# Optimization experiments

Measured on AMD Instinct MI355X. Metric: run time of the kernel, lower is better.

Reference implementation:

```python
import jax, jax.numpy as jnp
import numpy as np

N = 500_000   # mesh vertices
M = 500_000   # non-manifold sample points
K = 4         # quad-mesh valence
WEIGHTS = [7000.0, 600.0, 10.0, 50.0, 30.0, 3.0]


def setup_inputs() -> dict:
    key = jax.random.key(0)
    ks = jax.random.split(key, 11)
    return {
        "manifold_pred": jax.random.normal(ks[0], (1, N), jnp.float32),
        "nonmanifold_pred": jax.random.normal(ks[1], (1, M), jnp.float32),
        "mnfld_grad": jax.random.normal(ks[2], (1, N, 3), jnp.float32),
        "nonmnfld_grad": jax.random.normal(ks[3], (1, M, 3), jnp.float32),
        "mnfld_hessian": jax.random.normal(ks[4], (1, N, 3, 3), jnp.float32),
        "mnfld_n_gt": jax.random.normal(ks[5], (1, N, 3), jnp.float32),
        "theta": jax.random.normal(ks[6], (1, N, 1), jnp.float32),
        "local_coord_u": jax.random.normal(ks[7], (1, N, 3), jnp.float32),
        "local_coord_v": jax.random.normal(ks[8], (1, N, 3), jnp.float32),
        "rot": jax.random.normal(ks[9], (N, K, 3, 3), jnp.float32),
        "neighbors": jax.random.randint(ks[10], (N, K), 0, N, jnp.int32),
    }


def reference(manifold_pred, nonmanifold_pred, mnfld_grad, nonmnfld_grad,
              mnfld_hessian, mnfld_n_gt, theta, local_coord_u, local_coord_v,
              rot, neighbors):
    H = mnfld_hessian[0]          # [N,3,3] per-vertex hessian
    n_gt = mnfld_n_gt[0]          # [N,3]

    # morse term: n^T H  (div_type == 'l1')
    morse = 0.5 * jnp.abs(jnp.einsum('nd,nde->ne', n_gt, H)).mean()

    sdf_term = jnp.abs(manifold_pred).mean()

    # eikonal over concatenated grads (morse path uses nonmnfld_grad when near_points is None)
    all_grads = jnp.concatenate([nonmnfld_grad, mnfld_grad], axis=-2)  # [1, M+N, 3]
    eikonal_term = jnp.abs(jnp.linalg.norm(all_grads, axis=2) - 1.0).mean()

    inter_term = jnp.exp(-100.0 * jnp.abs(nonmanifold_pred)).mean()

    # cross-field directions from theta
    u, v, th = local_coord_u[0], local_coord_v[0], theta[0]  # [N,3],[N,3],[N,1]
    va = u * jnp.cos(th) + v * jnp.sin(th)
    va = va / (jnp.linalg.norm(va, axis=-1, keepdims=True) + 1e-12)
    vb = -u * jnp.sin(th) + v * jnp.cos(th)
    vb = vb / (jnp.linalg.norm(vb, axis=-1, keepdims=True) + 1e-12)

    # per-vertex (v^T H) x v hessian alignment (single valence group covers all vertices)
    vaH = jnp.einsum('nd,nde->ne', va, H)
    vbH = jnp.einsum('nd,nde->ne', vb, H)
    h_alpha = jnp.abs(jnp.cross(vaH, va)).mean()
    h_beta = jnp.abs(jnp.cross(vbH, vb)).mean()
    theta_hessian_term = 0.5 * (h_alpha + h_beta)

    # neighbor consistency: rotate neighbor cross-field into vertex frame, dot products
    vaj = jnp.einsum('nkij,nkj->nki', rot, va[neighbors])  # [N,K,3]
    vbj = jnp.einsum('nkij,nkj->nki', rot, vb[neighbors])
    aa = jnp.abs(jnp.einsum('nd,nkd->nk', va, vaj))
    ab = jnp.abs(jnp.einsum('nd,nkd->nk', va, vbj))
    ba = jnp.abs(jnp.einsum('nd,nkd->nk', vb, vaj))
    bb = jnp.abs(jnp.einsum('nd,nkd->nk', vb, vbj))
    theta_neighbors_term = (aa + ab + ba + bb - 2.0).mean()

    w = WEIGHTS
    loss = (w[0] * sdf_term + w[1] * inter_term + w[3] * eikonal_term
            + w[5] * morse + w[2] * theta_hessian_term + w[4] * theta_neighbors_term)
    return jnp.stack([loss, sdf_term, inter_term, eikonal_term, morse,
                      theta_hessian_term, theta_neighbors_term])
```

## Files before the change

kernel.cpp:

```cpp
#include <hip/hip_runtime.h>
#include <math.h>

static constexpr int BLOCK = 256;
static constexpr int WAVES = BLOCK / 64;
static constexpr int KVAL = 4;
static constexpr int TILE = 512;

typedef float f4 __attribute__((ext_vector_type(4)));
typedef int i4 __attribute__((ext_vector_type(4)));
typedef unsigned int u4v __attribute__((ext_vector_type(4)));
union VV { u4v u4; _Float16 h[8]; };
union PQ { u4v u[3]; _Float16 h[24]; };

__device__ __forceinline__ void norm3(float x, float y, float z,
                                      float& ox, float& oy, float& oz) {
  float inv = 1.0f / (sqrtf(x * x + y * y + z * z) + 1e-12f);
  ox = x * inv; oy = y * inv; oz = z * inv;
}

template <int NV>
__device__ __forceinline__ void block_reduce(float (&p)[NV]) {
#pragma unroll
  for (int off = 32; off > 0; off >>= 1)
#pragma unroll
    for (int q = 0; q < NV; ++q) p[q] += __shfl_down(p[q], off, 64);
  __shared__ float sm[WAVES][NV];
  int wave = threadIdx.x >> 6, lane = threadIdx.x & 63;
  if (lane == 0)
#pragma unroll
    for (int q = 0; q < NV; ++q) sm[wave][q] = p[q];
  __syncthreads();
  if (threadIdx.x == 0) {
#pragma unroll
    for (int q = 0; q < NV; ++q) {
      float t = 0.f;
#pragma unroll
      for (int w = 1; w < WAVES; ++w) t += sm[w][q];
      p[q] += t;
    }
  }
}

__device__ __forceinline__ void stage_f(float* __restrict__ dst,
                                        const float* __restrict__ src, int nf) {
  int t = threadIdx.x;
  int nf4 = nf >> 2;
  const f4* s4 = (const f4*)src;
  f4* d4 = (f4*)dst;
  for (int i = t; i < nf4; i += BLOCK) d4[i] = s4[i];
  int rem = nf & 3;
  if (t < rem) dst[nf4 * 4 + t] = src[nf4 * 4 + t];
}

__global__ __launch_bounds__(BLOCK) void s1_kernel(
    const float* __restrict__ theta, const float* __restrict__ u,
    const float* __restrict__ v, u4v* __restrict__ vavb,
    u4v* __restrict__ pq0, u4v* __restrict__ pq1, u4v* __restrict__ pq2, int N,
    const float* __restrict__ pred, const float* __restrict__ pgrad,
    const float* __restrict__ mp, const float* __restrict__ grad,
    const float* __restrict__ H, const float* __restrict__ ngt,
    const float* __restrict__ rot,
    float* __restrict__ part1, int nb1, int M) {
  __shared__ float B[9216];
  int t = threadIdx.x;
  long base = (long)blockIdx.x * TILE;
  float p[5] = {0.f, 0.f, 0.f, 0.f, 0.f};

  int cntM = 0, cntN = 0;
  if (base < M) { long c = (long)M - base; cntM = c > TILE ? TILE : (int)c; }
  if (base < N) { long c = (long)N - base; cntN = c > TILE ? TILE : (int)c; }

  if (cntM > 0) stage_f(B, pgrad + 3 * base, 3 * cntM);
  if (cntN > 0) {
    stage_f(B + 1536, grad + 3 * base, 3 * cntN);
    stage_f(B + 3072, ngt + 3 * base, 3 * cntN);
  }
  __syncthreads();
  float ngt_r[2][3];
#pragma unroll
  for (int w = 0; w < 2; ++w) {
    int k = t + 256 * w;
    long i = base + k;
    if (k < cntM) {
      float gx = B[3 * k], gy = B[3 * k + 1], gz = B[3 * k + 2];
      p[1] += fabsf(sqrtf(gx * gx + gy * gy + gz * gz) - 1.0f);
      p[4] += __expf(-100.0f * fabsf(pred[i]));
    }
    if (k < cntN) {
      float gx = B[1536 + 3 * k], gy = B[1536 + 3 * k + 1], gz = B[1536 + 3 * k + 2];
      p[1] += fabsf(sqrtf(gx * gx + gy * gy + gz * gz) - 1.0f);
      p[0] += fabsf(mp[i]);
      ngt_r[w][0] = B[3072 + 3 * k];
      ngt_r[w][1] = B[3072 + 3 * k + 1];
      ngt_r[w][2] = B[3072 + 3 * k + 2];
    }
  }
  __syncthreads();

  if (cntN > 0) {
    stage_f(B, u + 3 * base, 3 * cntN);
    stage_f(B + 1536, v + 3 * base, 3 * cntN);
  }
  __syncthreads();
  float va_r[2][3], vb_r[2][3];
#pragma unroll
  for (int w = 0; w < 2; ++w) {
    int k = t + 256 * w;
    long i = base + k;
    if (k < cntN) {
      float s, c;
      __sincosf(theta[i], &s, &c);
      float ux = B[3 * k], uy = B[3 * k + 1], uz = B[3 * k + 2];
      float vx = B[1536 + 3 * k], vy = B[1536 + 3 * k + 1], vz = B[1536 + 3 * k + 2];
      norm3(ux * c + vx * s, uy * c + vy * s, uz * c + vz * s,
            va_r[w][0], va_r[w][1], va_r[w][2]);
      norm3(vx * c - ux * s, vy * c - uy * s, vz * c - uz * s,
            vb_r[w][0], vb_r[w][1], vb_r[w][2]);
      VV o;
      o.h[0] = (_Float16)va_r[w][0]; o.h[1] = (_Float16)va_r[w][1];
      o.h[2] = (_Float16)va_r[w][2];
      o.h[3] = (_Float16)vb_r[w][0]; o.h[4] = (_Float16)vb_r[w][1];
      o.h[5] = (_Float16)vb_r[w][2];
      o.h[6] = (_Float16)0.f; o.h[7] = (_Float16)0.f;
      vavb[i] = o.u4;
    }
  }
  __syncthreads();

  if (cntN > 0) stage_f(B, H + 9 * base, 9 * cntN);
  __syncthreads();
#pragma unroll
  for (int w = 0; w < 2; ++w) {
    int k = t + 256 * w;
    if (k < cntN) {
      float h[9];
#pragma unroll
      for (int q = 0; q < 9; ++q) h[q] = B[9 * k + q];
      float n0 = ngt_r[w][0], n1 = ngt_r[w][1], n2 = ngt_r[w][2];
      p[2] += fabsf(n0 * h[0] + n1 * h[3] + n2 * h[6]) +
              fabsf(n0 * h[1] + n1 * h[4] + n2 * h[7]) +
              fabsf(n0 * h[2] + n1 * h[5] + n2 * h[8]);
      const float* va = va_r[w];
      const float* vb = vb_r[w];
      float a0 = va[0] * h[0] + va[1] * h[3] + va[2] * h[6];
      float a1 = va[0] * h[1] + va[1] * h[4] + va[2] * h[7];
      float a2 = va[0] * h[2] + va[1] * h[5] + va[2] * h[8];
      float b0 = vb[0] * h[0] + vb[1] * h[3] + vb[2] * h[6];
      float b1 = vb[0] * h[1] + vb[1] * h[4] + vb[2] * h[7];
      float b2 = vb[0] * h[2] + vb[1] * h[5] + vb[2] * h[8];
      p[3] += fabsf(a1 * va[2] - a2 * va[1]) + fabsf(a2 * va[0] - a0 * va[2]) +
              fabsf(a0 * va[1] - a1 * va[0]) + fabsf(b1 * vb[2] - b2 * vb[1]) +
              fabsf(b2 * vb[0] - b0 * vb[2]) + fabsf(b0 * vb[1] - b1 * vb[0]);
    }
  }
  __syncthreads();

#pragma unroll
  for (int sp = 0; sp < 2; ++sp) {
    int cnt = cntN - 256 * sp;
    if (cnt > 256) cnt = 256;
    long sb = base + 256 * sp;
    if (cnt > 0) stage_f(B, rot + 36 * sb, 36 * cnt);
    __syncthreads();
    if (t < cnt) {
      long i = sb + t;
      const f4* rr = (const f4*)(B + 36 * t);
      float r[36];
#pragma unroll
      for (int q = 0; q < 9; ++q) {
        f4 x = rr[q];
        r[4 * q] = x.x; r[4 * q + 1] = x.y; r[4 * q + 2] = x.z; r[4 * q + 3] = x.w;
      }
      const float* va = va_r[sp];
      const float* vb = vb_r[sp];
      PQ o;
#pragma unroll
      for (int k = 0; k < KVAL; ++k) {
        const float* R = r + 9 * k;
#pragma unroll
        for (int j = 0; j < 3; ++j) {
          float pa = R[j] * va[0] + R[3 + j] * va[1] + R[6 + j] * va[2];
          float pb = R[j] * vb[0] + R[3 + j] * vb[1] + R[6 + j] * vb[2];
          o.h[6 * k + j] = (_Float16)pa;
          o.h[6 * k + 3 + j] = (_Float16)pb;
        }
      }
      pq0[i] = o.u[0]; pq1[i] = o.u[1]; pq2[i] = o.u[2];
    }
    __syncthreads();
  }

  block_reduce<5>(p);
  if (t == 0) {
#pragma unroll
    for (int q = 0; q < 5; ++q) part1[q * nb1 + blockIdx.x] = p[q];
  }
}

__global__ __launch_bounds__(BLOCK) void s3_kernel(
    const u4v* __restrict__ vavb, const u4v* __restrict__ pq0,
    const u4v* __restrict__ pq1, const u4v* __restrict__ pq2,
    const i4* __restrict__ nbr, float* __restrict__ part2, int N) {
  int n = blockIdx.x * BLOCK + threadIdx.x;
  float p[1] = {0.f};
  if (n < N) {
    i4 jj = nbr[n];
    int js[4] = {jj.x, jj.y, jj.z, jj.w};
    VV wn[4];
#pragma unroll
    for (int k = 0; k < KVAL; ++k) wn[k].u4 = vavb[js[k]];
    PQ o;
    o.u[0] = pq0[n]; o.u[1] = pq1[n]; o.u[2] = pq2[n];
    float nsum = 0.f;
#pragma unroll
    for (int k = 0; k < KVAL; ++k) {
      float pa0 = (float)o.h[6 * k],     pa1 = (float)o.h[6 * k + 1],
            pa2 = (float)o.h[6 * k + 2];
      float pb0 = (float)o.h[6 * k + 3], pb1 = (float)o.h[6 * k + 4],
            pb2 = (float)o.h[6 * k + 5];
      float aj0 = (float)wn[k].h[0], aj1 = (float)wn[k].h[1], aj2 = (float)wn[k].h[2];
      float bj0 = (float)wn[k].h[3], bj1 = (float)wn[k].h[4], bj2 = (float)wn[k].h[5];
      nsum += fabsf(pa0 * aj0 + pa1 * aj1 + pa2 * aj2) +
              fabsf(pa0 * bj0 + pa1 * bj1 + pa2 * bj2) +
              fabsf(pb0 * aj0 + pb1 * aj1 + pb2 * aj2) +
              fabsf(pb0 * bj0 + pb1 * bj1 + pb2 * bj2) - 2.0f;
    }
    p[0] = nsum;
  }
  block_reduce<1>(p);
  if (threadIdx.x == 0) part2[blockIdx.x] = p[0];
}

__global__ __launch_bounds__(BLOCK) void finalize_fast(
    const float* __restrict__ part1, int nb1, const float* __restrict__ part2,
    int nb2, float* __restrict__ out, int N, int M) {
  float s[6] = {0.f, 0.f, 0.f, 0.f, 0.f, 0.f};
  for (int b = threadIdx.x; b < nb1; b += BLOCK) {
#pragma unroll
    for (int q = 0; q < 5; ++q) s[q] += part1[q * nb1 + b];
  }
  for (int b = threadIdx.x; b < nb2; b += BLOCK) s[5] += part2[b];
  block_reduce<6>(s);
  if (threadIdx.x == 0) {
    float sdf = s[0] / (float)N;
    float eik = s[1] / (float)(N + M);
    float morse = 0.5f * s[2] / (3.0f * (float)N);
    float th = 0.5f * s[3] / (3.0f * (float)N);
    float inter = s[4] / (float)M;
    float nb = s[5] / ((float)N * (float)KVAL);
    float loss = 7000.0f * sdf + 600.0f * inter + 50.0f * eik + 3.0f * morse +
                 10.0f * th + 30.0f * nb;
    out[0] = loss; out[1] = sdf; out[2] = inter; out[3] = eik;
    out[4] = morse; out[5] = th; out[6] = nb;
  }
}

__device__ __forceinline__ void crossfield(const float* __restrict__ u,
                                           const float* __restrict__ v,
                                           const float* __restrict__ theta,
                                           int n, float va[3], float vb[3]) {
  float s, c;
  __sincosf(theta[n], &s, &c);
  float ux = u[3 * n], uy = u[3 * n + 1], uz = u[3 * n + 2];
  float vx = v[3 * n], vy = v[3 * n + 1], vz = v[3 * n + 2];
  norm3(ux * c + vx * s, uy * c + vy * s, uz * c + vz * s, va[0], va[1], va[2]);
  norm3(vx * c - ux * s, vy * c - uy * s, vz * c - uz * s, vb[0], vb[1], vb[2]);
}

__global__ __launch_bounds__(BLOCK) void vertex_kernel(
    const float* __restrict__ mp, const float* __restrict__ grad,
    const float* __restrict__ H, const float* __restrict__ ngt,
    const float* __restrict__ theta, const float* __restrict__ u,
    const float* __restrict__ v, const float* __restrict__ rot,
    const int* __restrict__ nbr, float* __restrict__ acc, int N) {
  int n = blockIdx.x * blockDim.x + threadIdx.x;
  float p[5] = {0.f, 0.f, 0.f, 0.f, 0.f};
  if (n < N) {
    float hh[9];
#pragma unroll
    for (int i = 0; i < 9; ++i) hh[i] = H[9 * (size_t)n + i];
    p[0] = fabsf(mp[n]);
    float gx = grad[3 * n], gy = grad[3 * n + 1], gz = grad[3 * n + 2];
    p[1] = fabsf(sqrtf(gx * gx + gy * gy + gz * gz) - 1.0f);
    float n0 = ngt[3 * n], n1 = ngt[3 * n + 1], n2 = ngt[3 * n + 2];
    p[2] = fabsf(n0 * hh[0] + n1 * hh[3] + n2 * hh[6]) +
           fabsf(n0 * hh[1] + n1 * hh[4] + n2 * hh[7]) +
           fabsf(n0 * hh[2] + n1 * hh[5] + n2 * hh[8]);
    float va[3], vb[3];
    crossfield(u, v, theta, n, va, vb);
    {
      float a0 = va[0] * hh[0] + va[1] * hh[3] + va[2] * hh[6];
      float a1 = va[0] * hh[1] + va[1] * hh[4] + va[2] * hh[7];
      float a2 = va[0] * hh[2] + va[1] * hh[5] + va[2] * hh[8];
      float b0 = vb[0] * hh[0] + vb[1] * hh[3] + vb[2] * hh[6];
      float b1 = vb[0] * hh[1] + vb[1] * hh[4] + vb[2] * hh[7];
      float b2 = vb[0] * hh[2] + vb[1] * hh[5] + vb[2] * hh[8];
      p[3] = fabsf(a1 * va[2] - a2 * va[1]) + fabsf(a2 * va[0] - a0 * va[2]) +
             fabsf(a0 * va[1] - a1 * va[0]) + fabsf(b1 * vb[2] - b2 * vb[1]) +
             fabsf(b2 * vb[0] - b0 * vb[2]) + fabsf(b0 * vb[1] - b1 * vb[0]);
    }
    float nsum = 0.f;
    const float* R = rot + (size_t)n * (KVAL * 9);
#pragma unroll
    for (int k = 0; k < KVAL; ++k) {
      int j = nbr[KVAL * (size_t)n + k];
      float vaj[3], vbj[3];
      crossfield(u, v, theta, j, vaj, vbj);
      float r0 = R[9 * k + 0], r1 = R[9 * k + 1], r2 = R[9 * k + 2];
      float r3 = R[9 * k + 3], r4 = R[9 * k + 4], r5 = R[9 * k + 5];
      float r6 = R[9 * k + 6], r7 = R[9 * k + 7], r8 = R[9 * k + 8];
      float wa0 = r0 * vaj[0] + r1 * vaj[1] + r2 * vaj[2];
      float wa1 = r3 * vaj[0] + r4 * vaj[1] + r5 * vaj[2];
      float wa2 = r6 * vaj[0] + r7 * vaj[1] + r8 * vaj[2];
      float wb0 = r0 * vbj[0] + r1 * vbj[1] + r2 * vbj[2];
      float wb1 = r3 * vbj[0] + r4 * vbj[1] + r5 * vbj[2];
      float wb2 = r6 * vbj[0] + r7 * vbj[1] + r8 * vbj[2];
      nsum += fabsf(va[0] * wa0 + va[1] * wa1 + va[2] * wa2) +
              fabsf(va[0] * wb0 + va[1] * wb1 + va[2] * wb2) +
              fabsf(vb[0] * wa0 + vb[1] * wa1 + vb[2] * wa2) +
              fabsf(vb[0] * wb0 + vb[1] * wb1 + vb[2] * wb2) - 2.0f;
    }
    p[4] = nsum;
  }
  block_reduce<5>(p);
  if (threadIdx.x == 0) {
    atomicAdd(&acc[0], p[0]); atomicAdd(&acc[1], p[1]); atomicAdd(&acc[2], p[2]);
    atomicAdd(&acc[3], p[3]); atomicAdd(&acc[4], p[4]);
  }
}

__global__ __launch_bounds__(BLOCK) void point_kernel(
    const float* __restrict__ pred, const float* __restrict__ grad,
    float* __restrict__ acc, int M) {
  int i = blockIdx.x * blockDim.x + threadIdx.x;
  float p[2] = {0.f, 0.f};
  if (i < M) {
    p[0] = __expf(-100.0f * fabsf(pred[i]));
    float gx = grad[3 * i], gy = grad[3 * i + 1], gz = grad[3 * i + 2];
    p[1] = fabsf(sqrtf(gx * gx + gy * gy + gz * gz) - 1.0f);
  }
  block_reduce<2>(p);
  if (threadIdx.x == 0) {
    atomicAdd(&acc[5], p[0]); atomicAdd(&acc[1], p[1]);
  }
}

__global__ void finalize_acc(const float* __restrict__ acc, float* __restrict__ out,
                             int N, int M) {
  if (threadIdx.x == 0 && blockIdx.x == 0) {
    float sdf = acc[0] / (float)N;
    float eik = acc[1] / (float)(N + M);
    float morse = 0.5f * acc[2] / (3.0f * (float)N);
    float th = 0.5f * acc[3] / (3.0f * (float)N);
    float nb = acc[4] / ((float)N * (float)KVAL);
    float inter = acc[5] / (float)M;
    float loss = 7000.0f * sdf + 600.0f * inter + 50.0f * eik + 3.0f * morse +
                 10.0f * th + 30.0f * nb;
    out[0] = loss; out[1] = sdf; out[2] = inter; out[3] = eik;
    out[4] = morse; out[5] = th; out[6] = nb;
  }
}

extern "C" void kernel_launch(void* const* d_in, const int* in_sizes, int n_in,
                              void* d_out, int out_size, void* d_ws, size_t ws_size,
                              hipStream_t stream) {
  const float* mp    = (const float*)d_in[0];
  const float* npred = (const float*)d_in[1];
  const float* grad  = (const float*)d_in[2];
  const float* ngrad = (const float*)d_in[3];
  const float* H     = (const float*)d_in[4];
  const float* ngt   = (const float*)d_in[5];
  const float* theta = (const float*)d_in[6];
  const float* u     = (const float*)d_in[7];
  const float* v     = (const float*)d_in[8];
  const float* rot   = (const float*)d_in[9];
  const int*   nbr   = (const int*)d_in[10];
  float* out = (float*)d_out;

  int N = in_sizes[0];
  int M = in_sizes[1];
  int mx = (N > M) ? N : M;
  int nb1 = (mx + TILE - 1) / TILE;
  int nb2 = (N + BLOCK - 1) / BLOCK;

  size_t off_vavb = 256;
  size_t off_pq0 = off_vavb + (size_t)N * 16;
  size_t off_pq1 = off_pq0 + (size_t)N * 16;
  size_t off_pq2 = off_pq1 + (size_t)N * 16;
  size_t off_p1 = off_pq2 + (size_t)N * 16;
  size_t off_p2 = off_p1 + (size_t)5 * nb1 * 4;
  size_t need = off_p2 + (size_t)nb2 * 4;

  if (ws_size >= need) {
    u4v* vavb    = (u4v*)((char*)d_ws + off_vavb);
    u4v* pq0     = (u4v*)((char*)d_ws + off_pq0);
    u4v* pq1     = (u4v*)((char*)d_ws + off_pq1);
    u4v* pq2     = (u4v*)((char*)d_ws + off_pq2);
    float* part1 = (float*)((char*)d_ws + off_p1);
    float* part2 = (float*)((char*)d_ws + off_p2);
    s1_kernel<<<nb1, BLOCK, 0, stream>>>(
        theta, u, v, vavb, pq0, pq1, pq2, N, npred, ngrad, mp, grad, H, ngt,
        rot, part1, nb1, M);
    s3_kernel<<<nb2, BLOCK, 0, stream>>>(
        vavb, pq0, pq1, pq2, (const i4*)nbr, part2, N);
    finalize_fast<<<1, BLOCK, 0, stream>>>(part1, nb1, part2, nb2, out, N, M);
  } else {
    float* acc = (float*)d_ws;
    (void)hipMemsetAsync(acc, 0, 6 * sizeof(float), stream);
    vertex_kernel<<<(N + BLOCK - 1) / BLOCK, BLOCK, 0, stream>>>(
        mp, grad, H, ngt, theta, u, v, rot, nbr, acc, N);
    point_kernel<<<(M + BLOCK - 1) / BLOCK, BLOCK, 0, stream>>>(npred, ngrad, acc, M);
    finalize_acc<<<1, 64, 0, stream>>>(acc, out, N, M);
  }
}
```

Measured before the change: 61.44 us.

## Stage all s1 inputs at once via direct global-to-LDS loads with smaller tile

Halves the per-block tile to one element per thread and stages every input stream (grads, normals, u, v, Hessian, rotations) into shared memory in a single phase, using the global_load_lds builtin for full tiles so data goes straight to LDS without passing through registers. This removes the multiple staged phases and their barriers, leaving one sync before compute. Scalars are loaded into registers early to overlap with staging. The cost is a larger LDS footprint per block (about 60 KB), which may limit how many blocks fit on a CU, and twice as many blocks, each producing its own partial sums.

```diff
diff --git a/kernel.cpp b/kernel.cpp
--- a/kernel.cpp
+++ b/kernel.cpp
@@ -4,13 +4,22 @@
 static constexpr int BLOCK = 256;
 static constexpr int WAVES = BLOCK / 64;
 static constexpr int KVAL = 4;
-static constexpr int TILE = 512;
+static constexpr int TILE = 256;
 
 typedef float f4 __attribute__((ext_vector_type(4)));
 typedef int i4 __attribute__((ext_vector_type(4)));
 typedef unsigned int u4v __attribute__((ext_vector_type(4)));
 union VV { u4v u4; _Float16 h[8]; };
 union PQ { u4v u[3]; _Float16 h[24]; };
+
+static constexpr int L_PG = 0, L_G = 768, L_NG = 1536, L_U = 2304, L_V = 3072,
+                     L_H = 3840, L_R = 6144, L_TOT = 15360;
+
+__device__ __forceinline__ void gld_lds16(const void* g, void* l) {
+  __builtin_amdgcn_global_load_lds(
+      (const __attribute__((address_space(1))) void*)g,
+      (__attribute__((address_space(3))) void*)l, 16, 0, 0);
+}
 
 __device__ __forceinline__ void norm3(float x, float y, float z,
                                       float& ox, float& oy, float& oz) {
@@ -61,7 +70,7 @@
     const float* __restrict__ H, const float* __restrict__ ngt,
     const float* __restrict__ rot,
     float* __restrict__ part1, int nb1, int M) {
-  __shared__ float B[9216];
+  __shared__ float B[L_TOT];
   int t = threadIdx.x;
   long base = (long)blockIdx.x * TILE;
   float p[5] = {0.f, 0.f, 0.f, 0.f, 0.f};
@@ -70,124 +79,101 @@
   if (base < M) { long c = (long)M - base; cntM = c > TILE ? TILE : (int)c; }
   if (base < N) { long c = (long)N - base; cntN = c > TILE ? TILE : (int)c; }
 
-  if (cntM > 0) stage_f(B, pgrad + 3 * base, 3 * cntM);
-  if (cntN > 0) {
-    stage_f(B + 1536, grad + 3 * base, 3 * cntN);
-    stage_f(B + 3072, ngt + 3 * base, 3 * cntN);
+  float prv = 0.f, mpv = 0.f, thv = 0.f;
+  if (t < cntM) prv = pred[base + t];
+  if (t < cntN) { mpv = mp[base + t]; thv = theta[base + t]; }
+
+  bool full = (cntM == TILE) && (cntN == TILE);
+  if (full) {
+    int wave = t >> 6, lane = t & 63;
+    const float* srcs[7] = {pgrad + 3 * base, grad + 3 * base, ngt + 3 * base,
+                            u + 3 * base,     v + 3 * base,    H + 9 * base,
+                            rot + 36 * base};
+    const int foff[7] = {L_PG, L_G, L_NG, L_U, L_V, L_H, L_R};
+    const int nchk[7] = {3, 3, 3, 3, 3, 9, 36};
+    int c = wave, cs = 0;
+#pragma unroll
+    for (int s = 0; s < 7; ++s) {
+      while (c < cs + nchk[s]) {
+        int boff = (c - cs) * 1024;
+        gld_lds16((const char*)srcs[s] + boff + lane * 16,
+                  (char*)&B[foff[s]] + boff);
+        c += WAVES;
+      }
+      cs += nchk[s];
+    }
+  } else {
+    if (cntM > 0) stage_f(B + L_PG, pgrad + 3 * base, 3 * cntM);
+    if (cntN > 0) {
+      stage_f(B + L_G, grad + 3 * base, 3 * cntN);
+      stage_f(B + L_NG, ngt + 3 * base, 3 * cntN);
+      stage_f(B + L_U, u + 3 * base, 3 * cntN);
+      stage_f(B + L_V, v + 3 * base, 3 * cntN);
+      stage_f(B + L_H, H + 9 * base, 9 * cntN);
+      stage_f(B + L_R, rot + 36 * base, 36 * cntN);
+    }
   }
   __syncthreads();
-  float ngt_r[2][3];
-#pragma unroll
-  for (int w = 0; w < 2; ++w) {
-    int k = t + 256 * w;
-    long i = base + k;
-    if (k < cntM) {
-      float gx = B[3 * k], gy = B[3 * k + 1], gz = B[3 * k + 2];
-      p[1] += fabsf(sqrtf(gx * gx + gy * gy + gz * gz) - 1.0f);
-      p[4] += __expf(-100.0f * fabsf(pred[i]));
-    }
-    if (k < cntN) {
-      float gx = B[1536 + 3 * k], gy = B[1536 + 3 * k + 1], gz = B[1536 + 3 * k + 2];
-      p[1] += fabsf(sqrtf(gx * gx + gy * gy + gz * gz) - 1.0f);
-      p[0] += fabsf(mp[i]);
-      ngt_r[w][0] = B[3072 + 3 * k];
-      ngt_r[w][1] = B[3072 + 3 * k + 1];
-      ngt_r[w][2] = B[3072 + 3 * k + 2];
-    }
-  }
-  __syncthreads();
-
-  if (cntN > 0) {
-    stage_f(B, u + 3 * base, 3 * cntN);
-    stage_f(B + 1536, v + 3 * base, 3 * cntN);
-  }
-  __syncthreads();
-  float va_r[2][3], vb_r[2][3];
-#pragma unroll
-  for (int w = 0; w < 2; ++w) {
-    int k = t + 256 * w;
-    long i = base + k;
-    if (k < cntN) {
-      float s, c;
-      __sincosf(theta[i], &s, &c);
-      float ux = B[3 * k], uy = B[3 * k + 1], uz = B[3 * k + 2];
-      float vx = B[1536 + 3 * k], vy = B[1536 + 3 * k + 1], vz = B[1536 + 3 * k + 2];
-      norm3(ux * c + vx * s, uy * c + vy * s, uz * c + vz * s,
-            va_r[w][0], va_r[w][1], va_r[w][2]);
-      norm3(vx * c - ux * s, vy * c - uy * s, vz * c - uz * s,
-            vb_r[w][0], vb_r[w][1], vb_r[w][2]);
-      VV o;
-      o.h[0] = (_Float16)va_r[w][0]; o.h[1] = (_Float16)va_r[w][1];
-      o.h[2] = (_Float16)va_r[w][2];
-      o.h[3] = (_Float16)vb_r[w][0]; o.h[4] = (_Float16)vb_r[w][1];
-      o.h[5] = (_Float16)vb_r[w][2];
-      o.h[6] = (_Float16)0.f; o.h[7] = (_Float16)0.f;
-      vavb[i] = o.u4;
-    }
-  }
-  __syncthreads();
-
-  if (cntN > 0) stage_f(B, H + 9 * base, 9 * cntN);
-  __syncthreads();
-#pragma unroll
-  for (int w = 0; w < 2; ++w) {
-    int k = t + 256 * w;
-    if (k < cntN) {
-      float h[9];
-#pragma unroll
-      for (int q = 0; q < 9; ++q) h[q] = B[9 * k + q];
-      float n0 = ngt_r[w][0], n1 = ngt_r[w][1], n2 = ngt_r[w][2];
-      p[2] += fabsf(n0 * h[0] + n1 * h[3] + n2 * h[6]) +
-              fabsf(n0 * h[1] + n1 * h[4] + n2 * h[7]) +
-              fabsf(n0 * h[2] + n1 * h[5] + n2 * h[8]);
-      const float* va = va_r[w];
-      const float* vb = vb_r[w];
+
+  if (t < cntM) {
+    float gx = B[L_PG + 3 * t], gy = B[L_PG + 3 * t + 1], gz = B[L_PG + 3 * t + 2];
+    p[1] += fabsf(sqrtf(gx * gx + gy * gy + gz * gz) - 1.0f);
+    p[4] += __expf(-100.0f * fabsf(prv));
+  }
+  if (t < cntN) {
+    long i = base + t;
+    p[0] = fabsf(mpv);
+    float gx = B[L_G + 3 * t], gy = B[L_G + 3 * t + 1], gz = B[L_G + 3 * t + 2];
+    p[1] += fabsf(sqrtf(gx * gx + gy * gy + gz * gz) - 1.0f);
+
+    float s, cth;
+    __sincosf(thv, &s, &cth);
+    float ux = B[L_U + 3 * t], uy = B[L_U + 3 * t + 1], uz = B[L_U + 3 * t + 2];
+    float vx = B[L_V + 3 * t], vy = B[L_V + 3 * t + 1], vz = B[L_V + 3 * t + 2];
+    float va[3], vb[3];
+    norm3(ux * cth + vx * s, uy * cth + vy * s, uz * cth + vz * s,
+          va[0], va[1], va[2]);
+    norm3(vx * cth - ux * s, vy * cth - uy * s, vz * cth - uz * s,
+          vb[0], vb[1], vb[2]);
+    VV o;
+    o.h[0] = (_Float16)va[0]; o.h[1] = (_Float16)va[1]; o.h[2] = (_Float16)va[2];
+    o.h[3] = (_Float16)vb[0]; o.h[4] = (_Float16)vb[1]; o.h[5] = (_Float16)vb[2];
+    o.h[6] = (_Float16)0.f;   o.h[7] = (_Float16)0.f;
+    vavb[i] = o.u4;
+
+    float h[9];
+#pragma unroll
+    for (int q = 0; q < 9; ++q) h[q] = B[L_H + 9 * t + q];
+    float n0 = B[L_NG + 3 * t], n1 = B[L_NG + 3 * t + 1], n2 = B[L_NG + 3 * t + 2];
+    p[2] = fabsf(n0 * h[0] + n1 * h[3] + n2 * h[6]) +
+           fabsf(n0 * h[1] + n1 * h[4] + n2 * h[7]) +
+           fabsf(n0 * h[2] + n1 * h[5] + n2 * h[8]);
+    {
       float a0 = va[0] * h[0] + va[1] * h[3] + va[2] * h[6];
       float a1 = va[0] * h[1] + va[1] * h[4] + va[2] * h[7];
       float a2 = va[0] * h[2] + va[1] * h[5] + va[2] * h[8];
       float b0 = vb[0] * h[0] + vb[1] * h[3] + vb[2] * h[6];
       float b1 = vb[0] * h[1] + vb[1] * h[4] + vb[2] * h[7];
       float b2 = vb[0] * h[2] + vb[1] * h[5] + vb[2] * h[8];
-      p[3] += fabsf(a1 * va[2] - a2 * va[1]) + fabsf(a2 * va[0] - a0 * va[2]) +
-              fabsf(a0 * va[1] - a1 * va[0]) + fabsf(b1 * vb[2] - b2 * vb[1]) +
-              fabsf(b2 * vb[0] - b0 * vb[2]) + fabsf(b0 * vb[1] - b1 * vb[0]);
-    }
-  }
-  __syncthreads();
-
-#pragma unroll
-  for (int sp = 0; sp < 2; ++sp) {
-    int cnt = cntN - 256 * sp;
-    if (cnt > 256) cnt = 256;
-    long sb = base + 256 * sp;
-    if (cnt > 0) stage_f(B, rot + 36 * sb, 36 * cnt);
-    __syncthreads();
-    if (t < cnt) {
-      long i = sb + t;
-      const f4* rr = (const f4*)(B + 36 * t);
-      float r[36];
-#pragma unroll
-      for (int q = 0; q < 9; ++q) {
-        f4 x = rr[q];
-        r[4 * q] = x.x; r[4 * q + 1] = x.y; r[4 * q + 2] = x.z; r[4 * q + 3] = x.w;
+      p[3] = fabsf(a1 * va[2] - a2 * va[1]) + fabsf(a2 * va[0] - a0 * va[2]) +
+             fabsf(a0 * va[1] - a1 * va[0]) + fabsf(b1 * vb[2] - b2 * vb[1]) +
+             fabsf(b2 * vb[0] - b0 * vb[2]) + fabsf(b0 * vb[1] - b1 * vb[0]);
+    }
+    PQ o2;
+#pragma unroll
+    for (int k = 0; k < KVAL; ++k) {
+      float R[9];
+#pragma unroll
+      for (int q = 0; q < 9; ++q) R[q] = B[L_R + 36 * t + 9 * k + q];
+#pragma unroll
+      for (int j = 0; j < 3; ++j) {
+        float pa = R[j] * va[0] + R[3 + j] * va[1] + R[6 + j] * va[2];
+        float pb = R[j] * vb[0] + R[3 + j] * vb[1] + R[6 + j] * vb[2];
+        o2.h[6 * k + j] = (_Float16)pa;
+        o2.h[6 * k + 3 + j] = (_Float16)pb;
       }
-      const float* va = va_r[sp];
-      const float* vb = vb_r[sp];
-      PQ o;
-#pragma unroll
-      for (int k = 0; k < KVAL; ++k) {
-        const float* R = r + 9 * k;
-#pragma unroll
-        for (int j = 0; j < 3; ++j) {
-          float pa = R[j] * va[0] + R[3 + j] * va[1] + R[6 + j] * va[2];
-          float pb = R[j] * vb[0] + R[3 + j] * vb[1] + R[6 + j] * vb[2];
-          o.h[6 * k + j] = (_Float16)pa;
-          o.h[6 * k + 3 + j] = (_Float16)pb;
-        }
-      }
-      pq0[i] = o.u[0]; pq1[i] = o.u[1]; pq2[i] = o.u[2];
-    }
-    __syncthreads();
+    }
+    pq0[i] = o2.u[0]; pq1[i] = o2.u[1]; pq2[i] = o2.u[2];
   }
 
   block_reduce<5>(p);
```

Result: slower. 65.01 us (+5.8%).
